# Performance work log

Measured on AMD Instinct MI355X. Metric: run time of the kernel, lower is better.

## Reference

```python
import jax, jax.numpy as jnp
import numpy as np

N = 2_000_000
F = 32  # feature_num
GH = GW = 256


def _bilinear_interpolate(grid, coords):
    # grid: [H, W, F], coords: [N, 2] in (0,1)
    W = grid.shape[1] - 1
    H = grid.shape[0] - 1
    x = coords[:, 0] * W
    y = coords[:, 1] * H
    x0 = x.astype(jnp.int32)
    y0 = y.astype(jnp.int32)
    xf = x % 1
    yf = y % 1
    x1 = jnp.minimum(x0 + 1, W)
    y1 = jnp.minimum(y0 + 1, H)
    tl = grid[y0, x0]  # [N, F]
    tr = grid[y0, x1]
    bl = grid[y1, x0]
    br = grid[y1, x1]
    top = (1 - xf)[:, None] * tl + xf[:, None] * tr
    bot = (1 - xf)[:, None] * bl + xf[:, None] * br
    return (1 - yf)[:, None] * top + yf[:, None] * bot


def setup_inputs() -> dict:
    key = jax.random.key(0)
    ks = jax.random.split(key, 16)
    inp = {
        "pos": jax.random.uniform(ks[0], (N, 2), dtype=jnp.float32),
        "dir": jax.random.uniform(ks[1], (N, 2), dtype=jnp.float32),
        # grids: randn * 10 as in the torch module
        "pos_grid": jax.random.normal(ks[2], (GH, GW, F), dtype=jnp.float32) * 10.0,
        "dir_grid": jax.random.normal(ks[3], (GH, GW, F), dtype=jnp.float32) * 10.0,
        # shared encoder: Linear(2,4), Linear(4,3)
        "enc_w1": jax.random.normal(ks[4], (2, 4), dtype=jnp.float32) * 0.5,
        "enc_b1": jax.random.normal(ks[5], (4,), dtype=jnp.float32) * 0.1,
        "enc_w2": jax.random.normal(ks[6], (4, 3), dtype=jnp.float32) * 0.5,
        "enc_b2": jax.random.normal(ks[7], (3,), dtype=jnp.float32) * 0.1,
        # fc head: 2F -> 64 -> 16 -> 8 -> 3
        "fc_w1": jax.random.normal(ks[8], (2 * F, 64), dtype=jnp.float32) * 0.1,
        "fc_b1": jnp.zeros((64,), dtype=jnp.float32),
        "fc_w2": jax.random.normal(ks[9], (64, 16), dtype=jnp.float32) * 0.1,
        "fc_b2": jnp.zeros((16,), dtype=jnp.float32),
        "fc_w3": jax.random.normal(ks[10], (16, 8), dtype=jnp.float32) * 0.1,
        "fc_b3": jnp.zeros((8,), dtype=jnp.float32),
        "fc_w4": jax.random.normal(ks[11], (8, 3), dtype=jnp.float32) * 0.1,
        "fc_b4": jnp.zeros((3,), dtype=jnp.float32),
    }
    return inp


def reference(pos, dir, pos_grid, dir_grid,
              enc_w1, enc_b1, enc_w2, enc_b2,
              fc_w1, fc_b1, fc_w2, fc_b2, fc_w3, fc_b3, fc_w4, fc_b4):
    def encoder(x):
        h = jnp.tanh(x @ enc_w1 + enc_b1)
        return jax.nn.sigmoid(h @ enc_w2 + enc_b2)  # [N, 3]; only cols 0,1 used

    p = encoder(pos)
    d = encoder(dir)
    # features are .detach()'ed in the original
    pos_feat = jax.lax.stop_gradient(_bilinear_interpolate(pos_grid, p))
    dir_feat = jax.lax.stop_gradient(_bilinear_interpolate(dir_grid, d))
    x = jnp.concatenate([pos_feat, dir_feat], axis=1)  # [N, 2F]
    # Dropout layers are identity in eval mode
    x = jax.nn.leaky_relu(x @ fc_w1 + fc_b1)
    x = jax.nn.leaky_relu(x @ fc_w2 + fc_b2)
    x = jax.nn.leaky_relu(x @ fc_w3 + fc_b3)
    x = jax.nn.leaky_relu(x @ fc_w4 + fc_b4)
    return jax.nn.sigmoid(x) * 255.0
```

## Files before the change

kernel.cpp:

```cpp
#include <hip/hip_runtime.h>
#include <math.h>

typedef __attribute__((ext_vector_type(8))) __bf16 bf16x8;
typedef __attribute__((ext_vector_type(4))) __bf16 bf16x4;
typedef __attribute__((ext_vector_type(4))) float floatx4;
typedef __attribute__((ext_vector_type(8))) float floatx8;

__device__ __forceinline__ float fast_rcp(float x) { return __builtin_amdgcn_rcpf(x); }
__device__ __forceinline__ float sigmoidf_(float z) { return fast_rcp(1.0f + __expf(-z)); }
__device__ __forceinline__ float fast_tanh(float z) {
    float e = __expf(2.0f * z);
    return 1.0f - 2.0f * fast_rcp(e + 1.0f);
}
__device__ __forceinline__ float leaky(float v) { return fmaxf(v, 0.01f * v); }

__device__ __forceinline__ int swzb(int row, int byteoff) {
    return row * 128 + (byteoff ^ ((row & 7) << 4));
}

__global__ void convert_grids(const float* __restrict__ g0, const float* __restrict__ g1,
                              __bf16* __restrict__ o0, __bf16* __restrict__ o1, int elems) {
    int i = blockIdx.x * blockDim.x + threadIdx.x;
    int nvec = elems >> 2;
    if (i < nvec) {
        float4 v = ((const float4*)g0)[i];
        bf16x4 r = { (__bf16)v.x, (__bf16)v.y, (__bf16)v.z, (__bf16)v.w };
        ((bf16x4*)o0)[i] = r;
    } else if (i < 2 * nvec) {
        int j = i - nvec;
        float4 v = ((const float4*)g1)[j];
        bf16x4 r = { (__bf16)v.x, (__bf16)v.y, (__bf16)v.z, (__bf16)v.w };
        ((bf16x4*)o1)[j] = r;
    }
}

template<bool BF16G>
__global__ __launch_bounds__(256, 3) void gridnet_fwd(
    const float2* __restrict__ pos, const float2* __restrict__ dir_,
    const float* __restrict__ pos_gridf, const float* __restrict__ dir_gridf,
    const __bf16* __restrict__ pos_gridb, const __bf16* __restrict__ dir_gridb,
    const float* __restrict__ enc_w1, const float* __restrict__ enc_b1,
    const float* __restrict__ enc_w2, const float* __restrict__ enc_b2,
    const float* __restrict__ fc_w1, const float* __restrict__ fc_b1,
    const float* __restrict__ fc_w2, const float* __restrict__ fc_b2,
    const float* __restrict__ fc_w3, const float* __restrict__ fc_b3,
    const float* __restrict__ fc_w4, const float* __restrict__ fc_b4,
    float* __restrict__ out, int n)
{
    __shared__ __align__(1024) char smem[32768 + 8192 + 2048];
    __shared__ float b1lds[64];
    __shared__ float b2lds[16];

    const int tid  = threadIdx.x;
    const int lane = tid & 63;
    const int wid  = tid >> 6;
    const int quad = lane >> 4;
    const int l15  = lane & 15;

    char* Hw  = smem + wid * 8192;
    char* W1p = smem + 32768;
    char* W2p = smem + 32768 + 8192;

    for (int idx = tid; idx < 4096; idx += 256)
        *(__bf16*)(W1p + swzb(idx & 63, (idx >> 6) * 2)) = (__bf16)fc_w1[idx];
    for (int idx = tid; idx < 1024; idx += 256)
        *(__bf16*)(W2p + swzb(idx & 15, (idx >> 4) * 2)) = (__bf16)fc_w2[idx];
    if (tid < 64) b1lds[tid] = fc_b1[tid];
    if (tid < 16) b2lds[tid] = fc_b2[tid];
    __syncthreads();

    bf16x8 wf[2][4];
    #pragma unroll
    for (int ks = 0; ks < 2; ++ks)
        #pragma unroll
        for (int mt = 0; mt < 4; ++mt)
            wf[ks][mt] = *(const bf16x8*)(W1p + swzb(mt * 16 + l15, ks * 64 + quad * 16));
    floatx4 b1v[4];
    #pragma unroll
    for (int mt = 0; mt < 4; ++mt)
        b1v[mt] = *(const floatx4*)(b1lds + mt * 16 + quad * 4);

    int i  = blockIdx.x * 256 + wid * 64 + lane;
    int ic = min(i, n - 1);

    unsigned pcp[2];
    float xfp[2], yfp[2];
    #pragma unroll
    for (int pass = 0; pass < 2; ++pass) {
        float2 xy = pass ? dir_[ic] : pos[ic];
        float hh[4];
        #pragma unroll
        for (int k = 0; k < 4; ++k)
            hh[k] = fast_tanh(xy.x * enc_w1[k] + xy.y * enc_w1[4 + k] + enc_b1[k]);
        float e0 = enc_b2[0], e1 = enc_b2[1];
        #pragma unroll
        for (int k = 0; k < 4; ++k) {
            e0 += hh[k] * enc_w2[3 * k + 0];
            e1 += hh[k] * enc_w2[3 * k + 1];
        }
        float x = sigmoidf_(e0) * 255.0f;
        float y = sigmoidf_(e1) * 255.0f;
        int x0 = (int)x, y0 = (int)y;
        xfp[pass] = x - (float)x0;
        yfp[pass] = y - (float)y0;
        int x1 = min(x0 + 1, 255), y1 = min(y0 + 1, 255);
        pcp[pass] = (unsigned)x0 | ((unsigned)y0 << 8) | ((unsigned)x1 << 16) | ((unsigned)y1 << 24);
    }

    bf16x8 xfr[2][4];
    #pragma unroll
    for (int ks = 0; ks < 2; ++ks) {
        #pragma unroll
        for (int nt = 0; nt < 4; ++nt) {
            const int src = nt * 16 + l15;
            unsigned pcq = (unsigned)__shfl((int)pcp[ks], src);
            float xfq = __shfl(xfp[ks], src);
            float yfq = __shfl(yfp[ks], src);
            int x0 = pcq & 255, y0 = (pcq >> 8) & 255;
            int x1 = (pcq >> 16) & 255, y1 = pcq >> 24;
            float oxf = 1.0f - xfq, oyf = 1.0f - yfq;
            floatx8 r;
            if (BF16G) {
                const __bf16* ga = (ks ? dir_gridb : pos_gridb) + quad * 8;
                bf16x8 va = *(const bf16x8*)(ga + (((y0 << 8) + x0) << 5));
                bf16x8 vb = *(const bf16x8*)(ga + (((y0 << 8) + x1) << 5));
                bf16x8 vc = *(const bf16x8*)(ga + (((y1 << 8) + x0) << 5));
                bf16x8 vd = *(const bf16x8*)(ga + (((y1 << 8) + x1) << 5));
                r = (oyf * oxf) * __builtin_convertvector(va, floatx8)
                  + (oyf * xfq) * __builtin_convertvector(vb, floatx8)
                  + (yfq * oxf) * __builtin_convertvector(vc, floatx8)
                  + (yfq * xfq) * __builtin_convertvector(vd, floatx8);
            } else {
                const float* ga = (ks ? dir_gridf : pos_gridf) + quad * 8;
                floatx8 va = *(const floatx8*)(ga + (((y0 << 8) + x0) << 5));
                floatx8 vb = *(const floatx8*)(ga + (((y0 << 8) + x1) << 5));
                floatx8 vc = *(const floatx8*)(ga + (((y1 << 8) + x0) << 5));
                floatx8 vd = *(const floatx8*)(ga + (((y1 << 8) + x1) << 5));
                r = (oyf * oxf) * va + (oyf * xfq) * vb + (yfq * oxf) * vc + (yfq * xfq) * vd;
            }
            xfr[ks][nt] = __builtin_convertvector(r, bf16x8);
        }
    }

    floatx4 acc[4][4];
    #pragma unroll
    for (int mt = 0; mt < 4; ++mt)
        #pragma unroll
        for (int nt = 0; nt < 4; ++nt)
            acc[mt][nt] = b1v[mt];
    #pragma unroll
    for (int ks = 0; ks < 2; ++ks)
        #pragma unroll
        for (int mt = 0; mt < 4; ++mt)
            #pragma unroll
            for (int nt = 0; nt < 4; ++nt)
                acc[mt][nt] = __builtin_amdgcn_mfma_f32_16x16x32_bf16(wf[ks][mt], xfr[ks][nt], acc[mt][nt], 0, 0, 0);

    #pragma unroll
    for (int mt = 0; mt < 4; ++mt)
        #pragma unroll
        for (int nt = 0; nt < 4; ++nt) {
            bf16x4 hv;
            #pragma unroll
            for (int r = 0; r < 4; ++r)
                hv[r] = (__bf16)leaky(acc[mt][nt][r]);
            *(bf16x4*)(Hw + swzb(nt * 16 + l15, mt * 32 + quad * 8)) = hv;
        }
    __asm__ volatile("s_waitcnt lgkmcnt(0)" ::: "memory");

    bf16x8 w2f[2];
    #pragma unroll
    for (int ks = 0; ks < 2; ++ks)
        w2f[ks] = *(const bf16x8*)(W2p + swzb(l15, ks * 64 + quad * 16));
    floatx4 b2v = *(const floatx4*)(b2lds + quad * 4);
    floatx4 acc2[4];
    #pragma unroll
    for (int nt = 0; nt < 4; ++nt) acc2[nt] = b2v;
    #pragma unroll
    for (int ks = 0; ks < 2; ++ks) {
        #pragma unroll
        for (int nt = 0; nt < 4; ++nt) {
            bf16x8 hf = *(const bf16x8*)(Hw + swzb(nt * 16 + l15, ks * 64 + quad * 16));
            acc2[nt] = __builtin_amdgcn_mfma_f32_16x16x32_bf16(w2f[ks], hf, acc2[nt], 0, 0, 0);
        }
    }

    #pragma unroll
    for (int nt = 0; nt < 4; ++nt) {
        floatx4 hv;
        #pragma unroll
        for (int r = 0; r < 4; ++r)
            hv[r] = leaky(acc2[nt][r]);
        *(floatx4*)(Hw + swzb(nt * 16 + l15, quad * 16)) = hv;
    }
    __asm__ volatile("s_waitcnt lgkmcnt(0)" ::: "memory");

    float h2[16];
    #pragma unroll
    for (int c = 0; c < 4; ++c) {
        floatx4 v = *(const floatx4*)(Hw + swzb(lane, c * 16));
        h2[4 * c + 0] = v[0]; h2[4 * c + 1] = v[1]; h2[4 * c + 2] = v[2]; h2[4 * c + 3] = v[3];
    }
    float h3[8];
    #pragma unroll
    for (int j = 0; j < 8; ++j) h3[j] = fc_b3[j];
    #pragma unroll
    for (int k = 0; k < 16; ++k) {
        float xv = h2[k];
        #pragma unroll
        for (int j = 0; j < 8; ++j) h3[j] = fmaf(xv, fc_w3[(k << 3) + j], h3[j]);
    }
    #pragma unroll
    for (int j = 0; j < 8; ++j) h3[j] = leaky(h3[j]);

    float o[3];
    #pragma unroll
    for (int j = 0; j < 3; ++j) o[j] = fc_b4[j];
    #pragma unroll
    for (int k = 0; k < 8; ++k) {
        float xv = h3[k];
        #pragma unroll
        for (int j = 0; j < 3; ++j) o[j] = fmaf(xv, fc_w4[3 * k + j], o[j]);
    }
    if (i < n) {
        #pragma unroll
        for (int j = 0; j < 3; ++j)
            out[3 * i + j] = sigmoidf_(leaky(o[j])) * 255.0f;
    }
}

extern "C" void kernel_launch(void* const* d_in, const int* in_sizes, int n_in,
                              void* d_out, int out_size, void* d_ws, size_t ws_size,
                              hipStream_t stream) {
    int n = in_sizes[0] / 2;
    const int GELEMS = 256 * 256 * 32;
    bool use_bf16 = ws_size >= (size_t)(2 * GELEMS * sizeof(__bf16));
    __bf16* g0 = (__bf16*)d_ws;
    __bf16* g1 = g0 + GELEMS;

    if (use_bf16) {
        int total = 2 * (GELEMS / 4);
        convert_grids<<<(total + 255) / 256, 256, 0, stream>>>(
            (const float*)d_in[2], (const float*)d_in[3], g0, g1, GELEMS);
    }

    int blocks = (n + 255) / 256;
    if (use_bf16) {
        gridnet_fwd<true><<<blocks, 256, 0, stream>>>(
            (const float2*)d_in[0], (const float2*)d_in[1],
            (const float*)d_in[2], (const float*)d_in[3], g0, g1,
            (const float*)d_in[4], (const float*)d_in[5],
            (const float*)d_in[6], (const float*)d_in[7],
            (const float*)d_in[8], (const float*)d_in[9],
            (const float*)d_in[10], (const float*)d_in[11],
            (const float*)d_in[12], (const float*)d_in[13],
            (const float*)d_in[14], (const float*)d_in[15],
            (float*)d_out, n);
    } else {
        gridnet_fwd<false><<<blocks, 256, 0, stream>>>(
            (const float2*)d_in[0], (const float2*)d_in[1],
            (const float*)d_in[2], (const float*)d_in[3], g0, g1,
            (const float*)d_in[4], (const float*)d_in[5],
            (const float*)d_in[6], (const float*)d_in[7],
            (const float*)d_in[8], (const float*)d_in[9],
            (const float*)d_in[10], (const float*)d_in[11],
            (const float*)d_in[12], (const float*)d_in[13],
            (const float*)d_in[14], (const float*)d_in[15],
            (float*)d_out, n);
    }
}
```

Baseline: 218.0 us.

## Feed layer-1 MFMA output directly into layer-2 MFMA, shrink LDS for occupancy

Removes the LDS round-trip of the 64-wide hidden activation by reusing the layer-1 accumulator layout directly as the B operand of 16x16x16 bf16 MFMAs for layer 2, with the W2 fragments preloaded into registers. This cuts per-wave LDS scratch from 8 KB to 5 KB (a padded fp32 buffer), and launch bounds are raised from 3 to 5 blocks per SIMD to exploit the smaller footprint. Risks are register pressure under the tighter occupancy bound and using twice as many smaller-K MFMAs for layer 2.

```diff
diff --git a/kernel.cpp b/kernel.cpp
--- a/kernel.cpp
+++ b/kernel.cpp
@@ -3,6 +3,7 @@
 
 typedef __attribute__((ext_vector_type(8))) __bf16 bf16x8;
 typedef __attribute__((ext_vector_type(4))) __bf16 bf16x4;
+typedef __attribute__((ext_vector_type(4))) short short4v;
 typedef __attribute__((ext_vector_type(4))) float floatx4;
 typedef __attribute__((ext_vector_type(8))) float floatx8;
 
@@ -35,7 +36,7 @@
 }
 
 template<bool BF16G>
-__global__ __launch_bounds__(256, 3) void gridnet_fwd(
+__global__ __launch_bounds__(256, 5) void gridnet_fwd(
     const float2* __restrict__ pos, const float2* __restrict__ dir_,
     const float* __restrict__ pos_gridf, const float* __restrict__ dir_gridf,
     const __bf16* __restrict__ pos_gridb, const __bf16* __restrict__ dir_gridb,
@@ -47,7 +48,7 @@
     const float* __restrict__ fc_w4, const float* __restrict__ fc_b4,
     float* __restrict__ out, int n)
 {
-    __shared__ __align__(1024) char smem[32768 + 8192 + 2048];
+    __shared__ __align__(1024) char smem[8192 + 2048 + 4 * 5120];
     __shared__ float b1lds[64];
     __shared__ float b2lds[16];
 
@@ -57,9 +58,9 @@
     const int quad = lane >> 4;
     const int l15  = lane & 15;
 
-    char* Hw  = smem + wid * 8192;
-    char* W1p = smem + 32768;
-    char* W2p = smem + 32768 + 8192;
+    char* W1p = smem;
+    char* W2p = smem + 8192;
+    float* H2f = (float*)(smem + 10240 + wid * 5120);
 
     for (int idx = tid; idx < 4096; idx += 256)
         *(__bf16*)(W1p + swzb(idx & 63, (idx >> 6) * 2)) = (__bf16)fc_w1[idx];
@@ -75,10 +76,15 @@
         #pragma unroll
         for (int mt = 0; mt < 4; ++mt)
             wf[ks][mt] = *(const bf16x8*)(W1p + swzb(mt * 16 + l15, ks * 64 + quad * 16));
+    short4v w2a[4];
+    #pragma unroll
+    for (int kb = 0; kb < 4; ++kb)
+        w2a[kb] = *(const short4v*)(W2p + swzb(l15, kb * 32 + quad * 8));
     floatx4 b1v[4];
     #pragma unroll
     for (int mt = 0; mt < 4; ++mt)
         b1v[mt] = *(const floatx4*)(b1lds + mt * 16 + quad * 4);
+    floatx4 b2v = *(const floatx4*)(b2lds + quad * 4);
 
     int i  = blockIdx.x * 256 + wid * 64 + lane;
     int ic = min(i, n - 1);
@@ -156,32 +162,19 @@
             for (int nt = 0; nt < 4; ++nt)
                 acc[mt][nt] = __builtin_amdgcn_mfma_f32_16x16x32_bf16(wf[ks][mt], xfr[ks][nt], acc[mt][nt], 0, 0, 0);
 
-    #pragma unroll
-    for (int mt = 0; mt < 4; ++mt)
+    floatx4 acc2[4];
+    #pragma unroll
+    for (int nt = 0; nt < 4; ++nt) acc2[nt] = b2v;
+    #pragma unroll
+    for (int kb = 0; kb < 4; ++kb) {
         #pragma unroll
         for (int nt = 0; nt < 4; ++nt) {
             bf16x4 hv;
             #pragma unroll
             for (int r = 0; r < 4; ++r)
-                hv[r] = (__bf16)leaky(acc[mt][nt][r]);
-            *(bf16x4*)(Hw + swzb(nt * 16 + l15, mt * 32 + quad * 8)) = hv;
-        }
-    __asm__ volatile("s_waitcnt lgkmcnt(0)" ::: "memory");
-
-    bf16x8 w2f[2];
-    #pragma unroll
-    for (int ks = 0; ks < 2; ++ks)
-        w2f[ks] = *(const bf16x8*)(W2p + swzb(l15, ks * 64 + quad * 16));
-    floatx4 b2v = *(const floatx4*)(b2lds + quad * 4);
-    floatx4 acc2[4];
-    #pragma unroll
-    for (int nt = 0; nt < 4; ++nt) acc2[nt] = b2v;
-    #pragma unroll
-    for (int ks = 0; ks < 2; ++ks) {
-        #pragma unroll
-        for (int nt = 0; nt < 4; ++nt) {
-            bf16x8 hf = *(const bf16x8*)(Hw + swzb(nt * 16 + l15, ks * 64 + quad * 16));
-            acc2[nt] = __builtin_amdgcn_mfma_f32_16x16x32_bf16(w2f[ks], hf, acc2[nt], 0, 0, 0);
+                hv[r] = (__bf16)leaky(acc[kb][nt][r]);
+            acc2[nt] = __builtin_amdgcn_mfma_f32_16x16x16bf16_1k(
+                w2a[kb], __builtin_bit_cast(short4v, hv), acc2[nt], 0, 0, 0);
         }
     }
 
@@ -191,14 +184,14 @@
         #pragma unroll
         for (int r = 0; r < 4; ++r)
             hv[r] = leaky(acc2[nt][r]);
-        *(floatx4*)(Hw + swzb(nt * 16 + l15, quad * 16)) = hv;
+        *(floatx4*)(H2f + (nt * 16 + l15) * 20 + quad * 4) = hv;
     }
     __asm__ volatile("s_waitcnt lgkmcnt(0)" ::: "memory");
 
     float h2[16];
     #pragma unroll
     for (int c = 0; c < 4; ++c) {
-        floatx4 v = *(const floatx4*)(Hw + swzb(lane, c * 16));
+        floatx4 v = *(const floatx4*)(H2f + lane * 20 + c * 4);
         h2[4 * c + 0] = v[0]; h2[4 * c + 1] = v[1]; h2[4 * c + 2] = v[2]; h2[4 * c + 3] = v[3];
     }
     float h3[8];
```

New measurement: 285.0 us. +30.8%, slower.
